# Kernel optimization log

Hardware: AMD Instinct MI355X
Metric: run time of the kernel (lower is better)

## Reference

```python
import jax, jax.numpy as jnp
import numpy as np


def setup_inputs() -> dict:
    key = jax.random.key(0)
    inputs = jax.random.normal(key, (64, 2048, 512), dtype=jnp.float32)
    return {"inputs": inputs}


def reference(inputs) -> jnp.ndarray:
    # l2_type == 'one_by_one': squared L2 distance between consecutive timesteps,
    # with a leading 0, normalized per-sequence by the max distance.
    x = inputs.astype(jnp.float32)
    diffs = x[:, 1:] - x[:, :-1]                      # [B, S-1, D]
    d = jnp.sum(diffs * diffs, axis=-1)               # [B, S-1]
    B = x.shape[0]
    d = jnp.concatenate([jnp.zeros((B, 1), d.dtype), d], axis=1)  # [B, S]
    d = d / jnp.max(d, axis=1, keepdims=True)         # normalize by per-seq max
    return d
```

## Files before the change

### kernel.cpp

```cpp
#include <hip/hip_runtime.h>

#define NB 64
#define NS 2048
#define ND 512
#define TS 64
#define NWAVES 4
#define NCHUNK (NS / TS)

__global__ __launch_bounds__(256, 4) void l2_dist_kernel(const float* __restrict__ x,
                                                         float* __restrict__ out,
                                                         float* __restrict__ chunkmax) {
    const int b     = blockIdx.y;
    const int chunk = blockIdx.x;
    const int wave  = threadIdx.x >> 6;
    const int lane  = threadIdx.x & 63;

    __shared__ float wmaxes[NWAVES];

    const float* xb = x + (size_t)b * NS * ND;
    float wmax = 0.0f;

    #pragma unroll 4
    for (int i = 0; i < TS / NWAVES; ++i) {
        const int s = chunk * TS + i * NWAVES + wave;
        float sum = 0.0f;
        if (s > 0) {
            const float4* cur = (const float4*)(xb + (size_t)s * ND);
            const float4* prv = (const float4*)(xb + (size_t)(s - 1) * ND);
            float4 c0 = cur[lane];
            float4 p0 = prv[lane];
            float4 c1 = cur[lane + 64];
            float4 p1 = prv[lane + 64];
            float dx;
            dx = c0.x - p0.x; sum += dx * dx;
            dx = c0.y - p0.y; sum += dx * dx;
            dx = c0.z - p0.z; sum += dx * dx;
            dx = c0.w - p0.w; sum += dx * dx;
            dx = c1.x - p1.x; sum += dx * dx;
            dx = c1.y - p1.y; sum += dx * dx;
            dx = c1.z - p1.z; sum += dx * dx;
            dx = c1.w - p1.w; sum += dx * dx;
        }
        #pragma unroll
        for (int m = 32; m >= 1; m >>= 1)
            sum += __shfl_xor(sum, m, 64);
        if (lane == 0) out[(size_t)b * NS + s] = sum;
        wmax = fmaxf(wmax, sum);
    }

    if (lane == 0) wmaxes[wave] = wmax;
    __syncthreads();
    if (threadIdx.x == 0) {
        float m = wmaxes[0];
        #pragma unroll
        for (int w = 1; w < NWAVES; ++w) m = fmaxf(m, wmaxes[w]);
        chunkmax[b * NCHUNK + chunk] = m;
    }
}

__global__ __launch_bounds__(256) void l2_norm_kernel(float* __restrict__ out,
                                                      const float* __restrict__ chunkmax) {
    const int b    = blockIdx.y;
    const int half = blockIdx.x;
    const int tid  = threadIdx.x;

    __shared__ float smax;
    if (tid < 64) {
        float v = (tid < NCHUNK) ? chunkmax[b * NCHUNK + tid] : 0.0f;
        #pragma unroll
        for (int m = 16; m >= 1; m >>= 1)
            v = fmaxf(v, __shfl_xor(v, m, 64));
        if (tid == 0) smax = v;
    }
    __syncthreads();
    const float inv = 1.0f / smax;

    float4* row = (float4*)(out + (size_t)b * NS) + half * 256 + tid;
    float4 v = *row;
    v.x *= inv; v.y *= inv; v.z *= inv; v.w *= inv;
    *row = v;
}

extern "C" void kernel_launch(void* const* d_in, const int* in_sizes, int n_in,
                              void* d_out, int out_size, void* d_ws, size_t ws_size,
                              hipStream_t stream) {
    const float* x  = (const float*)d_in[0];
    float* out      = (float*)d_out;
    float* chunkmax = (float*)d_ws;

    l2_dist_kernel<<<dim3(NCHUNK, NB), dim3(256), 0, stream>>>(x, out, chunkmax);
    l2_norm_kernel<<<dim3(2, NB), dim3(256), 0, stream>>>(out, chunkmax);
}
```

Before: 359.7 us.

## Give each wave a run of consecutive rows and carry the previous row in registers

Each wavefront now handles 32 consecutive timesteps. It keeps the previous row's float4 values in registers instead of reloading row s-1 from global memory, which roughly halves global load traffic. Per-block shared-memory max reduction and __syncthreads are removed; each wave writes its own run max, and the norm kernel reduces 64 values per batch. The cost is fewer, longer-running waves with a serial dependency across rows, which may expose memory latency. The lane-to-column mapping also changes to two adjacent float4s per lane.

```diff
diff --git a/kernel.cpp b/kernel.cpp
--- a/kernel.cpp
+++ b/kernel.cpp
@@ -3,44 +3,45 @@
 #define NB 64
 #define NS 2048
 #define ND 512
-#define TS 64
-#define NWAVES 4
-#define NCHUNK (NS / TS)
+#define K  32
+#define WPB 4
+#define GPB (NS / K / WPB)
+#define NRUN (NS / K)
 
 __global__ __launch_bounds__(256, 4) void l2_dist_kernel(const float* __restrict__ x,
                                                          float* __restrict__ out,
-                                                         float* __restrict__ chunkmax) {
-    const int b     = blockIdx.y;
-    const int chunk = blockIdx.x;
-    const int wave  = threadIdx.x >> 6;
-    const int lane  = threadIdx.x & 63;
+                                                         float* __restrict__ runmax) {
+    const int b    = blockIdx.y;
+    const int wave = threadIdx.x >> 6;
+    const int lane = threadIdx.x & 63;
+    const int g    = blockIdx.x * WPB + wave;
+    const int s0   = g * K;
 
-    __shared__ float wmaxes[NWAVES];
+    const float4* xb = (const float4*)(x + (size_t)b * NS * ND);
+    const int RW = ND / 4;
+    const int c0 = lane * 2;
 
-    const float* xb = x + (size_t)b * NS * ND;
+    const int sp = (s0 > 0) ? s0 - 1 : 0;
+    float4 p0 = xb[(size_t)sp * RW + c0];
+    float4 p1 = xb[(size_t)sp * RW + c0 + 1];
+
     float wmax = 0.0f;
 
     #pragma unroll 4
-    for (int i = 0; i < TS / NWAVES; ++i) {
-        const int s = chunk * TS + i * NWAVES + wave;
-        float sum = 0.0f;
-        if (s > 0) {
-            const float4* cur = (const float4*)(xb + (size_t)s * ND);
-            const float4* prv = (const float4*)(xb + (size_t)(s - 1) * ND);
-            float4 c0 = cur[lane];
-            float4 p0 = prv[lane];
-            float4 c1 = cur[lane + 64];
-            float4 p1 = prv[lane + 64];
-            float dx;
-            dx = c0.x - p0.x; sum += dx * dx;
-            dx = c0.y - p0.y; sum += dx * dx;
-            dx = c0.z - p0.z; sum += dx * dx;
-            dx = c0.w - p0.w; sum += dx * dx;
-            dx = c1.x - p1.x; sum += dx * dx;
-            dx = c1.y - p1.y; sum += dx * dx;
-            dx = c1.z - p1.z; sum += dx * dx;
-            dx = c1.w - p1.w; sum += dx * dx;
-        }
+    for (int i = 0; i < K; ++i) {
+        const int s = s0 + i;
+        float4 c0v = xb[(size_t)s * RW + c0];
+        float4 c1v = xb[(size_t)s * RW + c0 + 1];
+        float dx, sum = 0.0f;
+        dx = c0v.x - p0.x; sum += dx * dx;
+        dx = c0v.y - p0.y; sum += dx * dx;
+        dx = c0v.z - p0.z; sum += dx * dx;
+        dx = c0v.w - p0.w; sum += dx * dx;
+        dx = c1v.x - p1.x; sum += dx * dx;
+        dx = c1v.y - p1.y; sum += dx * dx;
+        dx = c1v.z - p1.z; sum += dx * dx;
+        dx = c1v.w - p1.w; sum += dx * dx;
+        p0 = c0v; p1 = c1v;
         #pragma unroll
         for (int m = 32; m >= 1; m >>= 1)
             sum += __shfl_xor(sum, m, 64);
@@ -48,27 +49,20 @@
         wmax = fmaxf(wmax, sum);
     }
 
-    if (lane == 0) wmaxes[wave] = wmax;
-    __syncthreads();
-    if (threadIdx.x == 0) {
-        float m = wmaxes[0];
-        #pragma unroll
-        for (int w = 1; w < NWAVES; ++w) m = fmaxf(m, wmaxes[w]);
-        chunkmax[b * NCHUNK + chunk] = m;
-    }
+    if (lane == 0) runmax[b * NRUN + g] = wmax;
 }
 
 __global__ __launch_bounds__(256) void l2_norm_kernel(float* __restrict__ out,
-                                                      const float* __restrict__ chunkmax) {
+                                                      const float* __restrict__ runmax) {
     const int b    = blockIdx.y;
     const int half = blockIdx.x;
     const int tid  = threadIdx.x;
 
     __shared__ float smax;
     if (tid < 64) {
-        float v = (tid < NCHUNK) ? chunkmax[b * NCHUNK + tid] : 0.0f;
+        float v = runmax[b * NRUN + tid];
         #pragma unroll
-        for (int m = 16; m >= 1; m >>= 1)
+        for (int m = 32; m >= 1; m >>= 1)
             v = fmaxf(v, __shfl_xor(v, m, 64));
         if (tid == 0) smax = v;
     }
@@ -84,10 +78,10 @@
 extern "C" void kernel_launch(void* const* d_in, const int* in_sizes, int n_in,
                               void* d_out, int out_size, void* d_ws, size_t ws_size,
                               hipStream_t stream) {
-    const float* x  = (const float*)d_in[0];
-    float* out      = (float*)d_out;
-    float* chunkmax = (float*)d_ws;
+    const float* x = (const float*)d_in[0];
+    float* out     = (float*)d_out;
+    float* runmax  = (float*)d_ws;
 
-    l2_dist_kernel<<<dim3(NCHUNK, NB), dim3(256), 0, stream>>>(x, out, chunkmax);
-    l2_norm_kernel<<<dim3(2, NB), dim3(256), 0, stream>>>(out, chunkmax);
+    l2_dist_kernel<<<dim3(GPB, NB), dim3(256), 0, stream>>>(x, out, runmax);
+    l2_norm_kernel<<<dim3(2, NB), dim3(256), 0, stream>>>(out, runmax);
 }
```

After: 356.0 us. Within noise of the previous version (-1.0%).
